# Optimization experiments

Measured on AMD Instinct MI355X. Metric: run time of the kernel, lower is better.

The kernel has to match this reference:

```python
import jax, jax.numpy as jnp
import numpy as np

NODES = 81
NODE_DIM = 2
IN_DIM = NODES * NODE_DIM  # 162
D = 256
H = 16
HD = D // H
DFF = 2048
T, B, E = 1024, 8, 648


def _layernorm(x, w, b, eps=1e-5):
    m = x.mean(-1, keepdims=True)
    v = x.var(-1, keepdims=True)
    return (x - m) / jnp.sqrt(v + eps) * w + b


def setup_inputs() -> dict:
    key = jax.random.key(0)
    ks = jax.random.split(key, 12)
    s = 0.02
    W = lambda k, shape: jax.random.normal(k, shape, jnp.float32) * s
    return {
        "src": jax.random.normal(ks[0], (T, B, IN_DIM), jnp.float32),
        "edge_index": jax.random.randint(ks[1], (2, E), 0, NODES),
        "gcn_w": W(ks[2], (NODE_DIM, NODE_DIM)),
        "gcn_b": jnp.zeros((NODE_DIM,), jnp.float32),
        "fc_w": W(ks[3], (IN_DIM, D)),
        "fc_b": jnp.zeros((D,), jnp.float32),
        "wq": W(ks[4], (D, D)), "bq": jnp.zeros((D,), jnp.float32),
        "wk": W(ks[5], (D, D)), "bk": jnp.zeros((D,), jnp.float32),
        "wv": W(ks[6], (D, D)), "bv": jnp.zeros((D,), jnp.float32),
        "wo": W(ks[7], (D, D)), "bo": jnp.zeros((D,), jnp.float32),
        "ln1_w": jnp.ones((D,), jnp.float32), "ln1_b": jnp.zeros((D,), jnp.float32),
        "ffn_w1": W(ks[8], (D, DFF)), "ffn_b1": jnp.zeros((DFF,), jnp.float32),
        "ffn_w2": W(ks[9], (DFF, D)), "ffn_b2": jnp.zeros((D,), jnp.float32),
        "ln2_w": jnp.ones((D,), jnp.float32), "ln2_b": jnp.zeros((D,), jnp.float32),
        "dec_w": W(ks[10], (D, IN_DIM)), "dec_b": jnp.zeros((IN_DIM,), jnp.float32),
    }


def reference(src, edge_index, gcn_w, gcn_b, fc_w, fc_b, wq, bq, wk, bk, wv, bv,
              wo, bo, ln1_w, ln1_b, ffn_w1, ffn_b1, ffn_w2, ffn_b2, ln2_w, ln2_b,
              dec_w, dec_b):
    t, b, _ = src.shape
    # ---- batched GCNConv(2,2): all T*B tiny graphs share one adjacency ----
    # src[t,b] = [in_flow(81), out_flow(81)] -> node features [81, 2]
    xg = jnp.swapaxes(src.reshape(t, b, NODE_DIM, NODES), -1, -2)  # [T,B,81,2]
    row, col = edge_index[0], edge_index[1]
    A = jnp.zeros((NODES, NODES), src.dtype).at[col, row].add(1.0)
    A = A + jnp.eye(NODES, dtype=src.dtype)          # add self-loops
    deg = A.sum(1)
    dinv = jnp.where(deg > 0, 1.0 / jnp.sqrt(deg), 0.0)
    A_hat = dinv[:, None] * A * dinv[None, :]        # D^-1/2 (A+I) D^-1/2
    hg = jnp.einsum('ij,tbjc->tbic', A_hat, xg @ gcn_w) + gcn_b  # [T,B,81,2]
    # gcn_output.transpose(0,1).view(-1): channel-major flatten
    src2 = jnp.swapaxes(hg, -1, -2).reshape(t, b, IN_DIM)
    # ---- fc + positional encoding ----
    x = src2 @ fc_w + fc_b  # [T,B,D]
    pos = jnp.arange(t, dtype=jnp.float32)[:, None]
    div = jnp.exp(jnp.arange(0, D, 2, dtype=jnp.float32) * (-np.log(10000.0) / D))
    pe = jnp.zeros((t, D), x.dtype).at[:, 0::2].set(jnp.sin(pos * div))
    pe = pe.at[:, 1::2].set(jnp.cos(pos * div))
    x = x + pe[:, None, :]
    # ---- TransformerEncoderLayer (post-norm, relu, causal mask, eval) ----
    q = (x @ wq + bq).reshape(t, b, H, HD)
    k = (x @ wk + bk).reshape(t, b, H, HD)
    v = (x @ wv + bv).reshape(t, b, H, HD)
    scores = jnp.einsum('tbhd,sbhd->bhts', q, k) / jnp.sqrt(jnp.asarray(HD, x.dtype))
    causal = jnp.tril(jnp.ones((t, t), bool))
    scores = jnp.where(causal, scores, jnp.finfo(x.dtype).min)
    attn = jax.nn.softmax(scores, axis=-1)
    ctx = jnp.einsum('bhts,sbhd->tbhd', attn, v).reshape(t, b, D) @ wo + bo
    x = _layernorm(x + ctx, ln1_w, ln1_b)
    ff = jax.nn.relu(x @ ffn_w1 + ffn_b1) @ ffn_w2 + ffn_b2
    x = _layernorm(x + ff, ln2_w, ln2_b)
    return x @ dec_w + dec_b  # [T,B,162]
```

## Files before the change

### kernel.cpp

```cpp
#include <hip/hip_runtime.h>
#include <math.h>

#define T_    1024
#define B_    8
#define D_    256
#define H_    16
#define HD_   16
#define DFF_  2048
#define NODES_ 81
#define INDIM_ 162
#define E_    648
#define M_    (T_*B_)

typedef __bf16 bf16x8 __attribute__((ext_vector_type(8)));
typedef float  f32x4  __attribute__((ext_vector_type(4)));
typedef unsigned short ushort_t;
typedef unsigned int   uint_t;

union bfpack { bf16x8 v; uint_t u[4]; };

__device__ __forceinline__ ushort_t f2bf(float f) {
    union { float f; uint_t u; } c; c.f = f;
    uint_t u = c.u;
    uint_t r = u + 0x7fffu + ((u >> 16) & 1u);
    return (ushort_t)(r >> 16);
}

__device__ __forceinline__ uint_t fbits(float f) {
    union { float f; uint_t u; } c; c.f = f;
    return c.u;
}

__device__ __forceinline__ bf16x8 zero8() {
    bf16x8 v;
#pragma unroll
    for (int e = 0; e < 8; e++) v[e] = (__bf16)0.0f;
    return v;
}

__device__ __forceinline__ void gload_lds16(const void* g, void* l) {
    __builtin_amdgcn_global_load_lds(
        (const __attribute__((address_space(1))) void*)g,
        (__attribute__((address_space(3))) void*)l, 16, 0, 0);
}

__device__ __forceinline__ void trans_tile(
        const float* __restrict__ in, ushort_t* __restrict__ out,
        float (*tile)[33], int K, int N, int Kp, int bx, int by) {
    int k0 = bx * 32, n0 = by * 32;
    int tx = threadIdx.x & 31, ty = threadIdx.x >> 5;
#pragma unroll
    for (int i = 0; i < 4; i++) {
        int r = k0 + ty + i * 8, c = n0 + tx;
        tile[ty + i * 8][tx] = (r < K && c < N) ? in[(size_t)r * N + c] : 0.f;
    }
    __syncthreads();
#pragma unroll
    for (int i = 0; i < 4; i++) {
        int r = n0 + ty + i * 8, c = k0 + tx;
        out[(size_t)r * Kp + c] = f2bf(tile[tx][ty + i * 8]);
    }
}

__global__ __launch_bounds__(256) void prep_all(
        const int* __restrict__ edge, const float* __restrict__ gcn_w,
        const float* __restrict__ gcn_b, const float* __restrict__ fc_w,
        const float* __restrict__ fc_b, const float* __restrict__ src,
        const float* __restrict__ wq, const float* __restrict__ wk,
        const float* __restrict__ wv, const float* __restrict__ wo,
        const float* __restrict__ dec_w, const float* __restrict__ w1,
        const float* __restrict__ w2,
        const float* __restrict__ bq, const float* __restrict__ bk,
        const float* __restrict__ bv,
        ushort_t* __restrict__ weffT, float* __restrict__ beff,
        ushort_t* __restrict__ srcb,
        ushort_t* __restrict__ wqkvT, ushort_t* __restrict__ woT,
        ushort_t* __restrict__ dwT, ushort_t* __restrict__ w1T,
        ushort_t* __restrict__ w2T, float* __restrict__ qkvbias) {
    __shared__ float A[NODES_ * NODES_];
    __shared__ float dinv[NODES_];
    __shared__ float tile[32][33];
    int bid = blockIdx.x;
    int tid = threadIdx.x;
    if (bid < 82) {
        for (int i = tid; i < NODES_ * NODES_; i += 256) A[i] = 0.f;
        __syncthreads();
        for (int e = tid; e < E_; e += 256) {
            int r = edge[e];
            int c = edge[E_ + e];
            atomicAdd(&A[c * NODES_ + r], 1.0f);
        }
        __syncthreads();
        if (tid < NODES_) A[tid * NODES_ + tid] += 1.0f;
        __syncthreads();
        if (tid < NODES_) {
            float s = 0.f;
            for (int k = 0; k < NODES_; k++) s += A[tid * NODES_ + k];
            dinv[tid] = (s > 0.f) ? rsqrtf(s) : 0.f;
        }
        __syncthreads();
        int d = tid, j = bid;
        if (j < NODES_) {
            float s0 = 0.f, s1 = 0.f;
            for (int i = 0; i < NODES_; i++) {
                float a = dinv[i] * A[i * NODES_ + j] * dinv[j];
                s0 += a * fc_w[(0 * NODES_ + i) * D_ + d];
                s1 += a * fc_w[(1 * NODES_ + i) * D_ + d];
            }
            weffT[d * 192 + j]          = f2bf(gcn_w[0] * s0 + gcn_w[1] * s1);
            weffT[d * 192 + NODES_ + j] = f2bf(gcn_w[2] * s0 + gcn_w[3] * s1);
        } else {
            float t0 = 0.f, t1 = 0.f;
            for (int i = 0; i < NODES_; i++) {
                t0 += fc_w[(0 * NODES_ + i) * D_ + d];
                t1 += fc_w[(1 * NODES_ + i) * D_ + d];
            }
            beff[d] = fc_b[d] + gcn_b[0] * t0 + gcn_b[1] * t1;
            for (int c = INDIM_; c < 192; c++) weffT[d * 192 + c] = 0;
        }
    } else if (bid < 1426) {
        int l = bid - 82;
        if (l < 64)        trans_tile(wq,    wqkvT,          tile, D_,   D_,     D_,   l & 7,  l >> 3);
        else if (l < 128)  trans_tile(wk,    wqkvT + 65536,  tile, D_,   D_,     D_,   (l-64) & 7,  (l-64) >> 3);
        else if (l < 192)  trans_tile(wv,    wqkvT + 131072, tile, D_,   D_,     D_,   (l-128) & 7, (l-128) >> 3);
        else if (l < 256)  trans_tile(wo,    woT,            tile, D_,   D_,     D_,   (l-192) & 7, (l-192) >> 3);
        else if (l < 320)  trans_tile(dec_w, dwT,            tile, D_,   INDIM_, D_,   (l-256) & 7, (l-256) >> 3);
        else if (l < 832)  trans_tile(w1,    w1T,            tile, D_,   DFF_,   D_,   (l-320) & 7, (l-320) >> 3);
        else               trans_tile(w2,    w2T,            tile, DFF_, D_,     DFF_, (l-832) & 63, (l-832) >> 6);
    } else if (bid == 1426) {
#pragma unroll
        for (int k = 0; k < 3; k++) {
            int i = k * 256 + tid;
            qkvbias[i] = (i < 256) ? bq[i] : ((i < 512) ? bk[i - 256] : bv[i - 512]);
        }
    } else {
        int r = bid - 1427;
        if (tid < 192)
            srcb[(size_t)r * 192 + tid] =
                (tid < INDIM_) ? f2bf(src[(size_t)r * INDIM_ + tid]) : (ushort_t)0;
    }
}

enum { EP_PE = 0, EP_QKV = 1, EP_PLAIN = 2, EP_RELU = 3, EP_DEC = 4, EP_PART = 5 };

template <int EPI, int TM, int KS>
__global__ __launch_bounds__(256) void gemm_bf16(
        const ushort_t* __restrict__ A, const ushort_t* __restrict__ BT,
        const float* __restrict__ bias, float* __restrict__ Cf,
        ushort_t* __restrict__ Cb, int M, int N, int K) {
    __shared__ ushort_t sA[TM * 64];
    __shared__ ushort_t sB[128 * 64];
    int tid = threadIdx.x;
    int w = tid >> 6, lane = tid & 63;
    int cc = lane & 15, q = lane >> 4;
    int bm = blockIdx.y * TM, bn = blockIdx.x * 128;
    int part = (KS > 1) ? blockIdx.z : 0;
    int kbeg = part * (K / KS), kend = kbeg + K / KS;

    int srow = (lane >> 3);
    int sslot = lane & 7;

    const int NJ = (TM == 128) ? 4 : 2;
    int mbase = (TM == 128) ? ((w >> 1) * 64) : 0;
    int nbase = (TM == 128) ? ((w & 1) * 64) : (w * 32);

    f32x4 acc[4][NJ];
#pragma unroll
    for (int i = 0; i < 4; i++)
#pragma unroll
        for (int j = 0; j < NJ; j++)
#pragma unroll
            for (int e = 0; e < 4; e++) acc[i][j][e] = 0.f;

    for (int k0 = kbeg; k0 < kend; k0 += 64) {
        if (TM == 128) {
#pragma unroll
            for (int i = 0; i < 4; i++) {
                int r = w * 32 + i * 8 + srow;
                const ushort_t* ga = A + (size_t)(bm + r) * K + k0 + ((sslot ^ (r & 7)) * 8);
                gload_lds16(ga, &sA[(w * 32 + i * 8) * 64]);
            }
        } else {
#pragma unroll
            for (int i = 0; i < 2; i++) {
                int r = w * 16 + i * 8 + srow;
                const ushort_t* ga = A + (size_t)(bm + r) * K + k0 + ((sslot ^ (r & 7)) * 8);
                gload_lds16(ga, &sA[(w * 16 + i * 8) * 64]);
            }
        }
#pragma unroll
        for (int i = 0; i < 4; i++) {
            int r = w * 32 + i * 8 + srow;
            const ushort_t* gb = BT + (size_t)(bn + r) * K + k0 + ((sslot ^ (r & 7)) * 8);
            gload_lds16(gb, &sB[(w * 32 + i * 8) * 64]);
        }
        __syncthreads();
#pragma unroll
        for (int ks = 0; ks < 2; ks++) {
            bf16x8 af[4], bfr[NJ];
#pragma unroll
            for (int i = 0; i < 4; i++) {
                int m = mbase + i * 16 + cc;
                int off = m * 64 + (((ks * 4 + q) ^ (cc & 7)) * 8);
                af[i] = *(const bf16x8*)&sA[off];
            }
#pragma unroll
            for (int j = 0; j < NJ; j++) {
                int n = nbase + j * 16 + cc;
                int off = n * 64 + (((ks * 4 + q) ^ (cc & 7)) * 8);
                bfr[j] = *(const bf16x8*)&sB[off];
            }
#pragma unroll
            for (int i = 0; i < 4; i++)
#pragma unroll
                for (int j = 0; j < NJ; j++)
                    acc[i][j] = __builtin_amdgcn_mfma_f32_16x16x32_bf16(af[i], bfr[j], acc[i][j], 0, 0, 0);
        }
        __syncthreads();
    }

#pragma unroll
    for (int i = 0; i < 4; i++) {
#pragma unroll
        for (int j = 0; j < NJ; j++) {
            int col = bn + nbase + j * 16 + cc;
            float bv = 0.f;
            if (EPI == EP_DEC) bv = (col < INDIM_) ? bias[col] : 0.f;
            else if (EPI != EP_PART) bv = bias[col];
#pragma unroll
            for (int reg = 0; reg < 4; reg++) {
                int row = bm + mbase + i * 16 + q * 4 + reg;
                float v = acc[i][j][reg] + bv;
                if (EPI == EP_PE) {
                    int t = row >> 3;
                    float freq = __expf((float)(col & ~1) * (-9.210340371976184f / 256.f));
                    float ang = (float)t * freq;
                    v += (col & 1) ? __cosf(ang) : __sinf(ang);
                    Cf[(size_t)row * N + col] = v;
                    Cb[(size_t)row * N + col] = f2bf(v);
                } else if (EPI == EP_QKV) {
                    int t = row >> 3, b = row & 7;
                    int nn = col & 255, which = col >> 8;
                    int h = nn >> 4, hd = nn & 15;
                    float vq = (which == 0) ? v * 0.25f : v;
                    Cb[(size_t)which * 2097152 +
                       ((size_t)((b * H_ + h) * T_ + t)) * HD_ + hd] = f2bf(vq);
                } else if (EPI == EP_PLAIN) {
                    Cf[(size_t)row * N + col] = v;
                } else if (EPI == EP_RELU) {
                    v = fmaxf(v, 0.f);
                    Cb[(size_t)row * N + col] = f2bf(v);
                } else if (EPI == EP_DEC) {
                    if (col < INDIM_) Cf[(size_t)row * INDIM_ + col] = v;
                } else if (EPI == EP_PART) {
                    Cf[(size_t)part * M * N + (size_t)row * N + col] = v;
                }
            }
        }
    }
}

__global__ __launch_bounds__(256) void attn_mfma(
        const ushort_t* __restrict__ Qb, const ushort_t* __restrict__ Kb,
        const ushort_t* __restrict__ Vb, float* __restrict__ partO,
        float* __restrict__ partL) {
    const int qc_of[20] = {0,1,2,2,3,3,4,4,4,5,5,5,6,6,6,6,7,7,7,7};
    const int kp_of[20] = {0,0,0,1,0,1,0,1,2,0,1,2,0,1,2,3,0,1,2,3};
    int slot = blockIdx.x;
    int qc = qc_of[slot], kp = kp_of[slot];
    int bh = blockIdx.y;
    int tid = threadIdx.x;
    int w = tid >> 6, lane = tid & 63;
    int cc = lane & 15, q = lane >> 4;
    int qb0 = qc * 128;
    int kbeg = kp * 4;
    int kend = 2 * (qc + 1);
    if (kend > kbeg + 4) kend = kbeg + 4;

    __shared__ ushort_t VTs[2][16 * 72];

    const ushort_t* Qp = Qb + (size_t)bh * (T_ * HD_);
    const ushort_t* Kp = Kb + (size_t)bh * (T_ * HD_);
    const ushort_t* Vp = Vb + (size_t)bh * (T_ * HD_);

    bf16x8 qf[2];
#pragma unroll
    for (int i = 0; i < 2; i++) {
        if (q < 2)
            qf[i] = *(const bf16x8*)&Qp[(size_t)(qb0 + w * 32 + i * 16 + cc) * HD_ + q * 8];
        else
            qf[i] = zero8();
    }

    bf16x8 ones8;
#pragma unroll
    for (int e = 0; e < 8; e++) ones8[e] = (__bf16)1.0f;

    f32x4 ot[2], ls[2];
#pragma unroll
    for (int i = 0; i < 2; i++)
#pragma unroll
        for (int e = 0; e < 4; e++) { ot[i][e] = 0.f; ls[i][e] = 0.f; }

    int qmaxw = qb0 + w * 32 + 31;

    for (int kb = kbeg; kb < kend; kb++) {
        ushort_t* vbuf = VTs[kb & 1];
        {
            int r = tid >> 2, c0 = (tid & 3) * 4;
            ushort4 vv = *(const ushort4*)&Vp[(size_t)(kb * 64 + r) * HD_ + c0];
            vbuf[(c0 + 0) * 72 + r] = vv.x;
            vbuf[(c0 + 1) * 72 + r] = vv.y;
            vbuf[(c0 + 2) * 72 + r] = vv.z;
            vbuf[(c0 + 3) * 72 + r] = vv.w;
        }
        __syncthreads();
        if (kb * 64 > qmaxw) continue;

        bf16x8 kf[4];
#pragma unroll
        for (int j = 0; j < 4; j++) {
            if (q < 2)
                kf[j] = *(const bf16x8*)&Kp[(size_t)(kb * 64 + j * 16 + cc) * HD_ + q * 8];
            else
                kf[j] = zero8();
        }

        f32x4 s[2][4];
#pragma unroll
        for (int j = 0; j < 4; j++)
#pragma unroll
            for (int i = 0; i < 2; i++) {
                f32x4 z;
#pragma unroll
                for (int e = 0; e < 4; e++) z[e] = 0.f;
                s[i][j] = __builtin_amdgcn_mfma_f32_16x16x32_bf16(kf[j], qf[i], z, 0, 0, 0);
            }

#pragma unroll
        for (int j = 0; j < 4; j++) {
            bfpack af;
            const uint_t* vt = (const uint_t*)&vbuf[cc * 72 + j * 16 + q * 4];
            af.u[0] = vt[0]; af.u[1] = vt[1]; af.u[2] = 0u; af.u[3] = 0u;
            int key0 = kb * 64 + j * 16 + q * 4;
#pragma unroll
            for (int i = 0; i < 2; i++) {
                float p0 = __expf(s[i][j][0]);
                float p1 = __expf(s[i][j][1]);
                float p2 = __expf(s[i][j][2]);
                float p3 = __expf(s[i][j][3]);
                if (kb * 64 + j * 16 + 15 > qb0 + w * 32 + i * 16) {
                    int qrow = qb0 + w * 32 + i * 16 + cc;
                    if (key0 + 0 > qrow) p0 = 0.f;
                    if (key0 + 1 > qrow) p1 = 0.f;
                    if (key0 + 2 > qrow) p2 = 0.f;
                    if (key0 + 3 > qrow) p3 = 0.f;
                }
                bfpack pf;
                pf.u[0] = (fbits(p0) >> 16) | (fbits(p1) & 0xffff0000u);
                pf.u[1] = (fbits(p2) >> 16) | (fbits(p3) & 0xffff0000u);
                pf.u[2] = 0u; pf.u[3] = 0u;
                ot[i] = __builtin_amdgcn_mfma_f32_16x16x32_bf16(af.v, pf.v, ot[i], 0, 0, 0);
                ls[i] = __builtin_amdgcn_mfma_f32_16x16x32_bf16(ones8, pf.v, ls[i], 0, 0, 0);
            }
        }
    }

    int base = (bh * 20 + slot) * 128;
#pragma unroll
    for (int i = 0; i < 2; i++) {
        int row = w * 32 + i * 16 + cc;
        *(f32x4*)&partO[((size_t)(base + row)) * 16 + q * 4] = ot[i];
        if (q == 0) partL[base + row] = ls[i][0];
    }
}

__global__ __launch_bounds__(256) void attn_reduce(
        const float* __restrict__ partO, const float* __restrict__ partL,
        ushort_t* __restrict__ ctxb) {
    const int cum[9] = {0, 1, 2, 4, 6, 9, 12, 16, 20};
    int qc = blockIdx.x, bh = blockIdx.y;
    int row = threadIdx.x >> 1, dh = threadIdx.x & 1;
    int p0 = cum[qc], p1 = cum[qc + 1];
    float o[8];
#pragma unroll
    for (int e = 0; e < 8; e++) o[e] = 0.f;
    float l = 0.f;
    for (int p = p0; p < p1; p++) {
        size_t base = ((size_t)bh * 20 + p) * 128 + row;
        const float4 a = *(const float4*)&partO[base * 16 + dh * 8];
        const float4 b4 = *(const float4*)&partO[base * 16 + dh * 8 + 4];
        o[0] += a.x; o[1] += a.y; o[2] += a.z; o[3] += a.w;
        o[4] += b4.x; o[5] += b4.y; o[6] += b4.z; o[7] += b4.w;
        l += partL[base];
    }
    float inv = 1.f / l;
    int t = qc * 128 + row, b = bh >> 4, h = bh & 15;
    ushort_t* op = ctxb + ((size_t)t * B_ + b) * D_ + h * HD_ + dh * 8;
    ushort4 u0, u1;
    u0.x = f2bf(o[0] * inv); u0.y = f2bf(o[1] * inv);
    u0.z = f2bf(o[2] * inv); u0.w = f2bf(o[3] * inv);
    u1.x = f2bf(o[4] * inv); u1.y = f2bf(o[5] * inv);
    u1.z = f2bf(o[6] * inv); u1.w = f2bf(o[7] * inv);
    *(ushort4*)&op[0] = u0;
    *(ushort4*)&op[4] = u1;
}

template <int NP, bool HASB>
__global__ __launch_bounds__(256) void ln_kernel(
        const float* __restrict__ X, const float* __restrict__ P0,
        const float* __restrict__ P1, const float* __restrict__ RB,
        const float* __restrict__ w, const float* __restrict__ b,
        float* __restrict__ out, ushort_t* __restrict__ outb) {
    int wv = threadIdx.x >> 6, lane = threadIdx.x & 63;
    int row = blockIdx.x * 4 + wv;
    int c = lane * 4;
    const float4 x4 = *(const float4*)&X[(size_t)row * D_ + c];
    const float4 p4 = *(const float4*)&P0[(size_t)row * D_ + c];
    float v0 = x4.x + p4.x, v1 = x4.y + p4.y, v2 = x4.z + p4.z, v3 = x4.w + p4.w;
    if (NP == 2) {
        const float4 q4 = *(const float4*)&P1[(size_t)row * D_ + c];
        v0 += q4.x; v1 += q4.y; v2 += q4.z; v3 += q4.w;
    }
    if (HASB) {
        const float4 r4 = *(const float4*)&RB[c];
        v0 += r4.x; v1 += r4.y; v2 += r4.z; v3 += r4.w;
    }
    float s  = v0 + v1 + v2 + v3;
    float sq = v0 * v0 + v1 * v1 + v2 * v2 + v3 * v3;
    for (int off = 32; off; off >>= 1) {
        s  += __shfl_xor(s, off);
        sq += __shfl_xor(sq, off);
    }
    float mean = s * (1.f / 256.f);
    float var  = sq * (1.f / 256.f) - mean * mean;
    float rstd = rsqrtf(var + 1e-5f);
    float o0 = (v0 - mean) * rstd * w[c + 0] + b[c + 0];
    float o1 = (v1 - mean) * rstd * w[c + 1] + b[c + 1];
    float o2 = (v2 - mean) * rstd * w[c + 2] + b[c + 2];
    float o3 = (v3 - mean) * rstd * w[c + 3] + b[c + 3];
    float4 o; o.x = o0; o.y = o1; o.z = o2; o.w = o3;
    *(float4*)&out[(size_t)row * D_ + c] = o;
    ushort4 ob;
    ob.x = f2bf(o0); ob.y = f2bf(o1); ob.z = f2bf(o2); ob.w = f2bf(o3);
    *(ushort4*)&outb[(size_t)row * D_ + c] = ob;
}

extern "C" void kernel_launch(void* const* d_in, const int* in_sizes, int n_in,
                              void* d_out, int out_size, void* d_ws, size_t ws_size,
                              hipStream_t stream) {
    (void)in_sizes; (void)n_in; (void)out_size; (void)ws_size;
    const float* src     = (const float*)d_in[0];
    const int*   edge    = (const int*)d_in[1];
    const float* gcn_w   = (const float*)d_in[2];
    const float* gcn_b   = (const float*)d_in[3];
    const float* fc_w    = (const float*)d_in[4];
    const float* fc_b    = (const float*)d_in[5];
    const float* wq      = (const float*)d_in[6];
    const float* bq      = (const float*)d_in[7];
    const float* wk      = (const float*)d_in[8];
    const float* bk      = (const float*)d_in[9];
    const float* wv      = (const float*)d_in[10];
    const float* bv      = (const float*)d_in[11];
    const float* wo      = (const float*)d_in[12];
    const float* bo      = (const float*)d_in[13];
    const float* ln1_w   = (const float*)d_in[14];
    const float* ln1_b   = (const float*)d_in[15];
    const float* ffn_w1  = (const float*)d_in[16];
    const float* ffn_b1  = (const float*)d_in[17];
    const float* ffn_w2  = (const float*)d_in[18];
    const float* ffn_b2  = (const float*)d_in[19];
    const float* ln2_w   = (const float*)d_in[20];
    const float* ln2_b   = (const float*)d_in[21];
    const float* dec_w   = (const float*)d_in[22];
    const float* dec_b   = (const float*)d_in[23];
    float* out = (float*)d_out;

    float* ws = (float*)d_ws;
    float* beff    = ws;
    float* qkvbias = ws + 256;
    float* x0      = ws + 1024;
    float* tmp     = x0  + 2097152;
    float* tmp2    = tmp + 2097152;
    float* x1      = tmp2 + 2097152;
    float* x2s     = x1  + 2097152;
    ushort_t* ub   = (ushort_t*)(ws + 10486784);
    ushort_t* srcb = ub;
    ushort_t* x0b  = ub + 1572864;
    ushort_t* x1b  = x0b + 2097152;
    ushort_t* x2b  = x1b + 2097152;
    ushort_t* ctxb = x2b + 2097152;
    ushort_t* hb   = ctxb + 2097152;
    ushort_t* qkvb = hb + 16777216;
    ushort_t* weffT= qkvb + 6291456;
    ushort_t* wqkvT= weffT + 49152;
    ushort_t* woT  = wqkvT + 196608;
    ushort_t* w1T  = woT + 65536;
    ushort_t* w2T  = w1T + 524288;
    ushort_t* dwT  = w2T + 524288;
    float* partO = (float*)hb;
    float* partL = partO + 5242880;

    prep_all<<<9619, 256, 0, stream>>>(edge, gcn_w, gcn_b, fc_w, fc_b, src,
                                       wq, wk, wv, wo, dec_w, ffn_w1, ffn_w2,
                                       bq, bk, bv, weffT, beff, srcb,
                                       wqkvT, woT, dwT, w1T, w2T, qkvbias);

    gemm_bf16<EP_PE, 64, 1><<<dim3(2, 128), 256, 0, stream>>>(srcb, weffT, beff, x0, x0b, M_, D_, 192);
    gemm_bf16<EP_QKV, 64, 1><<<dim3(6, 128), 256, 0, stream>>>(x0b, wqkvT, qkvbias, nullptr, qkvb, M_, 768, D_);
    attn_mfma<<<dim3(20, 128), 256, 0, stream>>>(qkvb, qkvb + 2097152, qkvb + 4194304, partO, partL);
    attn_reduce<<<dim3(8, 128), 256, 0, stream>>>(partO, partL, ctxb);
    gemm_bf16<EP_PLAIN, 64, 1><<<dim3(2, 128), 256, 0, stream>>>(ctxb, woT, bo, tmp, nullptr, M_, D_, D_);
    ln_kernel<1, false><<<2048, 256, 0, stream>>>(x0, tmp, nullptr, nullptr, ln1_w, ln1_b, x1, x1b);
    gemm_bf16<EP_RELU, 128, 1><<<dim3(16, 64), 256, 0, stream>>>(x1b, w1T, ffn_b1, nullptr, hb, M_, DFF_, D_);
    gemm_bf16<EP_PART, 64, 2><<<dim3(2, 128, 2), 256, 0, stream>>>(hb, w2T, nullptr, tmp, nullptr, M_, D_, DFF_);
    ln_kernel<2, true><<<2048, 256, 0, stream>>>(x1, tmp, tmp2, ffn_b2, ln2_w, ln2_b, x2s, x2b);
    gemm_bf16<EP_DEC, 64, 1><<<dim3(2, 128), 256, 0, stream>>>(x2b, dwT, dec_b, out, nullptr, M_, D_, D_);
}
```

Before: 235.2 us.

## Pack two key subtiles per PV MFMA, scalar row sums, coarser src conversion

In the attention kernel, each PV MFMA now takes two 16-key subtiles, filling the full K=32 input instead of zero-padding half of it. This halves the PV MFMA count. The row-sum MFMA against a ones vector is replaced by scalar adds plus two cross-lane shuffles at the end. The src-to-bf16 conversion in the prep kernel now handles 64 rows per block instead of one, cutting the grid from 9619 to 1555 blocks and reducing block launch overhead. The row sum now accumulates fp32 probabilities rather than bf16-rounded ones, which slightly changes numerics relative to the numerator.

```diff
diff --git a/kernel.cpp b/kernel.cpp
--- a/kernel.cpp
+++ b/kernel.cpp
@@ -134,10 +134,20 @@
             qkvbias[i] = (i < 256) ? bq[i] : ((i < 512) ? bk[i - 256] : bv[i - 512]);
         }
     } else {
-        int r = bid - 1427;
-        if (tid < 192)
-            srcb[(size_t)r * 192 + tid] =
-                (tid < INDIM_) ? f2bf(src[(size_t)r * INDIM_ + tid]) : (ushort_t)0;
+        int blk = bid - 1427;
+        size_t row0 = (size_t)blk * 64;
+        const float* sp = src + row0 * INDIM_;
+        ushort_t* dp = srcb + row0 * 192;
+        for (int i = tid; i < 64 * INDIM_; i += 256) {
+            int r = i / INDIM_;
+            int c = i - r * INDIM_;
+            dp[(size_t)r * 192 + c] = f2bf(sp[i]);
+        }
+        for (int i = tid; i < 64 * 30; i += 256) {
+            int r = i / 30;
+            int c = i - r * 30;
+            dp[(size_t)r * 192 + INDIM_ + c] = 0;
+        }
     }
 }
 
@@ -292,15 +302,14 @@
             qf[i] = zero8();
     }
 
-    bf16x8 ones8;
-#pragma unroll
-    for (int e = 0; e < 8; e++) ones8[e] = (__bf16)1.0f;
-
-    f32x4 ot[2], ls[2];
-#pragma unroll
-    for (int i = 0; i < 2; i++)
-#pragma unroll
-        for (int e = 0; e < 4; e++) { ot[i][e] = 0.f; ls[i][e] = 0.f; }
+    f32x4 ot[2];
+    float lsum[2];
+#pragma unroll
+    for (int i = 0; i < 2; i++) {
+        lsum[i] = 0.f;
+#pragma unroll
+        for (int e = 0; e < 4; e++) ot[i][e] = 0.f;
+    }
 
     int qmaxw = qb0 + w * 32 + 31;
 
@@ -338,30 +347,47 @@
             }
 
 #pragma unroll
-        for (int j = 0; j < 4; j++) {
+        for (int jj = 0; jj < 2; jj++) {
+            int j0 = jj * 2, j1 = j0 + 1;
             bfpack af;
-            const uint_t* vt = (const uint_t*)&vbuf[cc * 72 + j * 16 + q * 4];
-            af.u[0] = vt[0]; af.u[1] = vt[1]; af.u[2] = 0u; af.u[3] = 0u;
-            int key0 = kb * 64 + j * 16 + q * 4;
+            const uint_t* vt0 = (const uint_t*)&vbuf[cc * 72 + j0 * 16 + q * 4];
+            const uint_t* vt1 = (const uint_t*)&vbuf[cc * 72 + j1 * 16 + q * 4];
+            af.u[0] = vt0[0]; af.u[1] = vt0[1];
+            af.u[2] = vt1[0]; af.u[3] = vt1[1];
+            int key00 = kb * 64 + j0 * 16 + q * 4;
+            int key01 = key00 + 16;
 #pragma unroll
             for (int i = 0; i < 2; i++) {
-                float p0 = __expf(s[i][j][0]);
-                float p1 = __expf(s[i][j][1]);
-                float p2 = __expf(s[i][j][2]);
-                float p3 = __expf(s[i][j][3]);
-                if (kb * 64 + j * 16 + 15 > qb0 + w * 32 + i * 16) {
-                    int qrow = qb0 + w * 32 + i * 16 + cc;
-                    if (key0 + 0 > qrow) p0 = 0.f;
-                    if (key0 + 1 > qrow) p1 = 0.f;
-                    if (key0 + 2 > qrow) p2 = 0.f;
-                    if (key0 + 3 > qrow) p3 = 0.f;
+                float p0 = __expf(s[i][j0][0]);
+                float p1 = __expf(s[i][j0][1]);
+                float p2 = __expf(s[i][j0][2]);
+                float p3 = __expf(s[i][j0][3]);
+                float p4 = __expf(s[i][j1][0]);
+                float p5 = __expf(s[i][j1][1]);
+                float p6 = __expf(s[i][j1][2]);
+                float p7 = __expf(s[i][j1][3]);
+                int qsub = qb0 + w * 32 + i * 16;
+                if (kb * 64 + j0 * 16 + 15 > qsub) {
+                    int qrow = qsub + cc;
+                    if (key00 + 0 > qrow) p0 = 0.f;
+                    if (key00 + 1 > qrow) p1 = 0.f;
+                    if (key00 + 2 > qrow) p2 = 0.f;
+                    if (key00 + 3 > qrow) p3 = 0.f;
+                }
+                if (kb * 64 + j1 * 16 + 15 > qsub) {
+                    int qrow = qsub + cc;
+                    if (key01 + 0 > qrow) p4 = 0.f;
+                    if (key01 + 1 > qrow) p5 = 0.f;
+                    if (key01 + 2 > qrow) p6 = 0.f;
+                    if (key01 + 3 > qrow) p7 = 0.f;
                 }
                 bfpack pf;
                 pf.u[0] = (fbits(p0) >> 16) | (fbits(p1) & 0xffff0000u);
                 pf.u[1] = (fbits(p2) >> 16) | (fbits(p3) & 0xffff0000u);
-                pf.u[2] = 0u; pf.u[3] = 0u;
+                pf.u[2] = (fbits(p4) >> 16) | (fbits(p5) & 0xffff0000u);
+                pf.u[3] = (fbits(p6) >> 16) | (fbits(p7) & 0xffff0000u);
                 ot[i] = __builtin_amdgcn_mfma_f32_16x16x32_bf16(af.v, pf.v, ot[i], 0, 0, 0);
-                ls[i] = __builtin_amdgcn_mfma_f32_16x16x32_bf16(ones8, pf.v, ls[i], 0, 0, 0);
+                lsum[i] += ((p0 + p1) + (p2 + p3)) + ((p4 + p5) + (p6 + p7));
             }
         }
     }
@@ -369,9 +395,12 @@
     int base = (bh * 20 + slot) * 128;
 #pragma unroll
     for (int i = 0; i < 2; i++) {
+        float l = lsum[i];
+        l += __shfl_xor(l, 16);
+        l += __shfl_xor(l, 32);
         int row = w * 32 + i * 16 + cc;
         *(f32x4*)&partO[((size_t)(base + row)) * 16 + q * 4] = ot[i];
-        if (q == 0) partL[base + row] = ls[i][0];
+        if (q == 0) partL[base + row] = l;
     }
 }
 
@@ -501,7 +530,7 @@
     float* partO = (float*)hb;
     float* partL = partO + 5242880;
 
-    prep_all<<<9619, 256, 0, stream>>>(edge, gcn_w, gcn_b, fc_w, fc_b, src,
+    prep_all<<<1555, 256, 0, stream>>>(edge, gcn_w, gcn_b, fc_w, fc_b, src,
                                        wq, wk, wv, wo, dec_w, ffn_w1, ffn_w2,
                                        bq, bk, bv, weffT, beff, srcb,
                                        wqkvT, woT, dwT, w1T, w2T, qkvbias);
```

Result: no change. 238.3 us (+1.3%).
